# Performance work log

Measured on AMD Instinct MI355X. Metric: run time of the kernel, lower is better.

The kernel has to match this reference:

```python
import jax, jax.numpy as jnp
import numpy as np

B, S, D, H = 2, 2048, 1024, 16
DK = D // H


def setup_inputs() -> dict:
    key = jax.random.key(0)
    ks = jax.random.split(key, 9)
    def xavier(k, shape):
        fan_in, fan_out = shape[1], shape[0]
        lim = jnp.sqrt(6.0 / (fan_in + fan_out))
        return jax.random.uniform(k, shape, jnp.float32, -lim, lim)
    x = jax.random.normal(ks[0], (B, S, D), jnp.float32)
    mask = jnp.ones((B, 1, S), jnp.int32)
    Wq = xavier(ks[1], (D, D)); bq = jnp.zeros((D,), jnp.float32)
    Wk = xavier(ks[2], (D, D)); bk = jnp.zeros((D,), jnp.float32)
    Wv = xavier(ks[3], (D, D)); bv = jnp.zeros((D,), jnp.float32)
    Wo = xavier(ks[4], (D, D)); bo = jnp.zeros((D,), jnp.float32)
    return {"x": x, "mask": mask, "Wq": Wq, "bq": bq, "Wk": Wk, "bk": bk,
            "Wv": Wv, "bv": bv, "Wo": Wo, "bo": bo}


def reference(x, mask, Wq, bq, Wk, bk, Wv, bv, Wo, bo):
    # Linear layers use torch convention y = x @ W.T + b
    q = (x @ Wq.T + bq).reshape(B, S, H, DK).transpose(0, 2, 1, 3)  # [B,H,S,DK]
    k = (x @ Wk.T + bk).reshape(B, S, H, DK).transpose(0, 2, 1, 3)
    v = (x @ Wv.T + bv).reshape(B, S, H, DK).transpose(0, 2, 1, 3)
    scores = jnp.einsum('bhqd,bhkd->bhqk', q, k) / jnp.sqrt(jnp.float32(DK))
    m = mask[:, None, :, :]  # unsqueeze(1): broadcast over heads -> [B,1,1,S]
    scores = jnp.where(m == 0, jnp.float32(-1e9), scores)
    p = jax.nn.softmax(scores, axis=-1)  # dropout p=0.0 -> identity
    ctx = jnp.einsum('bhqk,bhkd->bhqd', p, v)
    ctx = ctx.transpose(0, 2, 1, 3).reshape(B, S, D)
    return ctx @ Wo.T + bo
```

## Files before the change

kernel.cpp:

```cpp
#include <hip/hip_runtime.h>
#include <hip/hip_bf16.h>
#include <math.h>

#define Bn 2
#define Sn 2048
#define Dn 1024
#define Hn 16
#define DKn 64
#define BHS (Bn * Hn * Sn)

using fragb  = __attribute__((ext_vector_type(8))) short;
using frag16 = __attribute__((ext_vector_type(8))) _Float16;
using f4     = __attribute__((ext_vector_type(4))) float;

__device__ __forceinline__ short f2bf(float f) {
    union { float f; unsigned u; } v; v.f = f;
    unsigned r = v.u + 0x7FFF + ((v.u >> 16) & 1);
    return (short)(r >> 16);
}
__device__ __forceinline__ unsigned short f2h(float f) {
    _Float16 h = (_Float16)f;
    unsigned short s; __builtin_memcpy(&s, &h, 2); return s;
}

#define GLOAD(gptr, lptr)                                                     \
    __builtin_amdgcn_global_load_lds(                                         \
        (const __attribute__((address_space(1))) unsigned int*)(const void*)(gptr), \
        (__attribute__((address_space(3))) unsigned int*)(void*)(lptr), 16, 0, 0)

#define NX (Bn * Sn * Dn)
#define NW (Dn * Dn)
#define NF4 ((NX + 4 * NW) / 4)

__global__ __launch_bounds__(256) void prep(
    const float* __restrict__ x,  const float* __restrict__ Wq,
    const float* __restrict__ Wk, const float* __restrict__ Wv,
    const float* __restrict__ Wo, const int* __restrict__ mask,
    short* __restrict__ xh,
    short* __restrict__ Wqh, short* __restrict__ Wkh,
    short* __restrict__ Wvh, short* __restrict__ Woh,
    short* __restrict__ mfb)
{
    int i = blockIdx.x * 256 + threadIdx.x;
    if (i < NF4) {
        int e = i << 2;
        const float* src; short* dst; int j;
        if (e < NX)               { src = x;  dst = xh;  j = e; }
        else if (e < NX + NW)     { src = Wq; dst = Wqh; j = e - NX; }
        else if (e < NX + 2 * NW) { src = Wk; dst = Wkh; j = e - NX - NW; }
        else if (e < NX + 3 * NW) { src = Wv; dst = Wvh; j = e - NX - 2 * NW; }
        else                      { src = Wo; dst = Woh; j = e - NX - 3 * NW; }
        float4 v = *(const float4*)(src + j);
        ushort4 o;
        o.x = f2h(v.x); o.y = f2h(v.y); o.z = f2h(v.z); o.w = f2h(v.w);
        *(ushort4*)(dst + j) = o;
    } else {
        int j = (i - NF4) << 2;
        if (j < Bn * Sn) {
            int4 m = *(const int4*)(mask + j);
            ushort4 o;
            o.x = m.x ? 0x3F80 : 0; o.y = m.y ? 0x3F80 : 0;
            o.z = m.z ? 0x3F80 : 0; o.w = m.w ? 0x3F80 : 0;
            *(ushort4*)(mfb + j) = o;
        }
    }
}


#define STAGE(kk0) do {                                                       \
    const short* _as = Asrc + (kk0);                                          \
    const short* _bs = Bsrc + (kk0);                                          \
    GLOAD(_as,            &As[wave * 512]);                                   \
    GLOAD(_as + 32 * Dn,  &As[2048 + wave * 512]);                            \
    GLOAD(_as + 64 * Dn,  &As[4096 + wave * 512]);                            \
    GLOAD(_as + 96 * Dn,  &As[6144 + wave * 512]);                            \
    GLOAD(_bs,            &Bs[wave * 512]);                                   \
    GLOAD(_bs + 32 * Dn,  &Bs[2048 + wave * 512]);                            \
    GLOAD(_bs + 64 * Dn,  &Bs[4096 + wave * 512]);                            \
    GLOAD(_bs + 96 * Dn,  &Bs[6144 + wave * 512]);                            \
} while (0)

#define COMPUTE() do {                                                        \
    frag16 _a[2][4], _b[2][4];                                                \
    _Pragma("unroll")                                                         \
    for (int kk = 0; kk < 2; kk++) {                                          \
        _Pragma("unroll")                                                     \
        for (int mi = 0; mi < 4; mi++)                                        \
            _a[kk][mi] = *(const frag16*)&As[                                 \
                (wm * 64 + mi * 16 + l16) * 64 +                              \
                (((kk << 2) | quad) ^ (l16 & 7)) * 8];                        \
        _Pragma("unroll")                                                     \
        for (int ni = 0; ni < 4; ni++)                                        \
            _b[kk][ni] = *(const frag16*)&Bs[                                 \
                (wn * 64 + ni * 16 + l16) * 64 +                              \
                (((kk << 2) | quad) ^ (l16 & 7)) * 8];                        \
    }                                                                         \
    _Pragma("unroll")                                                         \
    for (int kk = 0; kk < 2; kk++)                                            \
        _Pragma("unroll")                                                     \
        for (int mi = 0; mi < 4; mi++)                                        \
            _Pragma("unroll")                                                 \
            for (int ni = 0; ni < 4; ni++)                                    \
                acc[mi][ni] = __builtin_amdgcn_mfma_f32_16x16x32_f16(         \
                    _a[kk][mi], _b[kk][ni], acc[kk ? mi : mi][ni], 0, 0, 0);  \
} while (0)

__global__ __launch_bounds__(256) void gemm_qkv(
    const short* __restrict__ A,
    const short* __restrict__ W0, const float* __restrict__ b0,
    const short* __restrict__ W1, const float* __restrict__ b1,
    const short* __restrict__ W2, const float* __restrict__ b2,
    const int* __restrict__ mask,
    short* __restrict__ Qb, short* __restrict__ Kb, short* __restrict__ Vtb)
{
    __shared__ __align__(16) short As[128 * 64];
    __shared__ __align__(16) short Bs[128 * 64];

    const int tid  = threadIdx.x;
    const int wave = tid >> 6;
    const int lane = tid & 63;
    const int quad = lane >> 4;
    const int l16  = lane & 15;
    const int wm   = wave >> 1;
    const int wn   = wave & 1;

    const int m0   = blockIdx.y * 128;
    const int n0   = blockIdx.x * 128;
    const int widx = n0 >> 10;
    const int nl0  = n0 & 1023;

    const short* Wp   = widx == 0 ? W0 : (widx == 1 ? W1 : W2);
    const float* bias = widx == 0 ? b0 : (widx == 1 ? b1 : b2);

    f4 acc[4][4];
    #pragma unroll
    for (int i = 0; i < 4; i++)
        #pragma unroll
        for (int j = 0; j < 4; j++) {
            acc[i][j][0] = 0.f; acc[i][j][1] = 0.f;
            acc[i][j][2] = 0.f; acc[i][j][3] = 0.f;
        }

    const int sr = tid >> 3;
    const int sc = ((tid & 7) ^ (sr & 7)) * 8;
    const short* Asrc = A  + (size_t)(m0  + sr) * Dn + sc;
    const short* Bsrc = Wp + (size_t)(nl0 + sr) * Dn + sc;

    for (int k0 = 0; k0 < Dn; k0 += 64) {
        __syncthreads();
        STAGE(k0);
        __syncthreads();
        COMPUTE();
    }

    const float QSCALE = 0.125f * 1.44269504088896340736f;

    #pragma unroll
    for (int mi = 0; mi < 4; mi++) {
        #pragma unroll
        for (int ni = 0; ni < 4; ni++) {
            int nl = nl0 + wn * 64 + ni * 16 + l16;
            float bv = bias[nl];
            #pragma unroll
            for (int r = 0; r < 4; r++) {
                int m = m0 + wm * 64 + mi * 16 + quad * 4 + r;
                float v = acc[mi][ni][r] + bv;
                int b  = m >> 11, s = m & (Sn - 1);
                int h  = nl >> 6, dk = nl & 63;
                if (widx == 0)
                    Qb[((size_t)(b * Hn + h) * Sn + s) * DKn + dk] = f2bf(v * QSCALE);
                else if (widx == 1)
                    Kb[((size_t)(b * Hn + h) * Sn + s) * DKn + dk] = f2bf(v);
                else {
                    float mv = (float)mask[b * Sn + s];
                    Vtb[((size_t)(b * Hn + h) * DKn + dk) * Sn + s] = f2bf(v * mv);
                }
            }
        }
    }
}

__global__ __launch_bounds__(256) void gemm_out(
    const short* __restrict__ A, const short* __restrict__ Wp,
    const float* __restrict__ bias, float* __restrict__ outf)
{
    __shared__ __align__(16) short As[128 * 64];
    __shared__ __align__(16) short Bs[128 * 64];

    const int tid  = threadIdx.x;
    const int wave = tid >> 6;
    const int lane = tid & 63;
    const int quad = lane >> 4;
    const int l16  = lane & 15;
    const int wm   = wave >> 1;
    const int wn   = wave & 1;

    const int m0 = blockIdx.y * 128;
    const int n0 = blockIdx.x * 128;

    f4 acc[4][4];
    #pragma unroll
    for (int i = 0; i < 4; i++)
        #pragma unroll
        for (int j = 0; j < 4; j++) {
            acc[i][j][0] = 0.f; acc[i][j][1] = 0.f;
            acc[i][j][2] = 0.f; acc[i][j][3] = 0.f;
        }

    const int sr = tid >> 3;
    const int sc = ((tid & 7) ^ (sr & 7)) * 8;
    const short* Asrc = A  + (size_t)(m0 + sr) * Dn + sc;
    const short* Bsrc = Wp + (size_t)(n0 + sr) * Dn + sc;

    for (int k0 = 0; k0 < Dn; k0 += 64) {
        __syncthreads();
        STAGE(k0);
        __syncthreads();
        COMPUTE();
    }

    #pragma unroll
    for (int mi = 0; mi < 4; mi++) {
        #pragma unroll
        for (int ni = 0; ni < 4; ni++) {
            int nl = n0 + wn * 64 + ni * 16 + l16;
            float bv = bias[nl];
            #pragma unroll
            for (int r = 0; r < 4; r++) {
                int m = m0 + wm * 64 + mi * 16 + quad * 4 + r;
                outf[(size_t)m * Dn + nl] = acc[mi][ni][r] + bv;
            }
        }
    }
}

#define LP  72

__global__ __launch_bounds__(256) void attn_mfma(
    const short* __restrict__ Qb, const short* __restrict__ Kb,
    const short* __restrict__ Vtb, const short* __restrict__ mfb,
    float* __restrict__ ctxp0, float* __restrict__ ctxp1,
    float* __restrict__ lp)
{
    __shared__ __align__(16) short Ks[64 * 64];
    __shared__ __align__(16) short Vs[64 * 64];
    __shared__ short Ps[4][32 * LP];
    __shared__ __align__(16) short mfs[64];

    const int tid  = threadIdx.x;
    const int wave = tid >> 6;
    const int lane = tid & 63;
    const int quad = lane >> 4;
    const int l16  = lane & 15;

    const int split = blockIdx.x & 1;
    const int rest  = blockIdx.x >> 1;
    const int qt  = rest & 15;
    const int bhh = rest >> 4;
    const int b   = bhh >> 4;
    const int h   = bhh & 15;

    fragb qf[2][2];
    #pragma unroll
    for (int w = 0; w < 2; w++) {
        int qrow = qt * 128 + wave * 32 + w * 16 + l16;
        const short* qptr = Qb + ((size_t)bhh * Sn + qrow) * DKn + quad * 8;
        qf[w][0] = *(const fragb*)(qptr);
        qf[w][1] = *(const fragb*)(qptr + 32);
    }

    f4 ctx[2][4];
    #pragma unroll
    for (int w = 0; w < 2; w++)
        #pragma unroll
        for (int dt = 0; dt < 4; dt++) {
            ctx[w][dt][0] = 0.f; ctx[w][dt][1] = 0.f;
            ctx[w][dt][2] = 0.f; ctx[w][dt][3] = 0.f;
        }
    f4 lacc[2];
    lacc[0][0] = 0.f; lacc[0][1] = 0.f; lacc[0][2] = 0.f; lacc[0][3] = 0.f;
    lacc[1] = lacc[0];

    const int lr = lane >> 3;
    const int sc = ((lane & 7) ^ lr) * 8;
    const short* Kg = Kb  + (size_t)bhh * Sn * DKn;
    const short* Vg = Vtb + (size_t)bhh * DKn * Sn;
    const short* mg = mfb + (size_t)b * Sn;

    const short* Ksrc = Kg + (size_t)(wave * 16 + lr) * DKn + sc;
    const short* Vsrc = Vg + (size_t)(wave * 16 + lr) * Sn + sc;

    const int c0 = ((quad ^ (l16 & 7)) * 8);

    const int kt0 = split * 16;
    for (int kt = kt0; kt < kt0 + 16; kt++) {
        __syncthreads();
        GLOAD(Ksrc + (size_t)kt * 4096,             &Ks[(wave * 16) * 64]);
        GLOAD(Ksrc + (size_t)kt * 4096 + 8 * DKn,   &Ks[(wave * 16 + 8) * 64]);
        GLOAD(Vsrc + (size_t)kt * 64,               &Vs[(wave * 16) * 64]);
        GLOAD(Vsrc + (size_t)kt * 64 + 8 * Sn,      &Vs[(wave * 16 + 8) * 64]);
        if (tid < 8)
            *(uint4*)&mfs[tid * 8] = *(const uint4*)(mg + kt * 64 + tid * 8);
        __syncthreads();

        #pragma unroll
        for (int t = 0; t < 4; t++) {
            fragb k0 = *(const fragb*)&Ks[(t * 16 + l16) * 64 + c0];
            fragb k1 = *(const fragb*)&Ks[(t * 16 + l16) * 64 + (c0 ^ 32)];
            #pragma unroll
            for (int w = 0; w < 2; w++) {
                f4 a; a[0] = 0.f; a[1] = 0.f; a[2] = 0.f; a[3] = 0.f;
                a = __builtin_amdgcn_mfma_f32_16x16x32_bf16(k0, qf[w][0], a, 0, 0, 0);
                a = __builtin_amdgcn_mfma_f32_16x16x32_bf16(k1, qf[w][1], a, 0, 0, 0);
                unsigned u0 = __float_as_uint(__builtin_amdgcn_exp2f(a[0]));
                unsigned u1 = __float_as_uint(__builtin_amdgcn_exp2f(a[1]));
                unsigned u2 = __float_as_uint(__builtin_amdgcn_exp2f(a[2]));
                unsigned u3 = __float_as_uint(__builtin_amdgcn_exp2f(a[3]));
                uint2 pw;
                pw.x = __builtin_amdgcn_perm(u1, u0, 0x07060302u);
                pw.y = __builtin_amdgcn_perm(u3, u2, 0x07060302u);
                *(uint2*)&Ps[wave][(w * 16 + l16) * LP + 16 * t + quad * 4] = pw;
            }
        }

        fragb p[2][2];
        #pragma unroll
        for (int w = 0; w < 2; w++) {
            p[w][0] = *(const fragb*)&Ps[wave][(w * 16 + l16) * LP + quad * 8];
            p[w][1] = *(const fragb*)&Ps[wave][(w * 16 + l16) * LP + quad * 8 + 32];
        }
        fragb m0 = *(const fragb*)&mfs[quad * 8];
        fragb m1 = *(const fragb*)&mfs[quad * 8 + 32];
        #pragma unroll
        for (int w = 0; w < 2; w++) {
            lacc[w] = __builtin_amdgcn_mfma_f32_16x16x32_bf16(p[w][0], m0, lacc[w], 0, 0, 0);
            lacc[w] = __builtin_amdgcn_mfma_f32_16x16x32_bf16(p[w][1], m1, lacc[w], 0, 0, 0);
        }
        #pragma unroll
        for (int dt = 0; dt < 4; dt++) {
            fragb v0 = *(const fragb*)&Vs[(dt * 16 + l16) * 64 + c0];
            fragb v1 = *(const fragb*)&Vs[(dt * 16 + l16) * 64 + (c0 ^ 32)];
            #pragma unroll
            for (int w = 0; w < 2; w++) {
                ctx[w][dt] = __builtin_amdgcn_mfma_f32_16x16x32_bf16(p[w][0], v0, ctx[w][dt], 0, 0, 0);
                ctx[w][dt] = __builtin_amdgcn_mfma_f32_16x16x32_bf16(p[w][1], v1, ctx[w][dt], 0, 0, 0);
            }
        }
    }

    float* cp  = split ? ctxp1 : ctxp0;
    float* lpp = lp + (size_t)split * BHS;
    #pragma unroll
    for (int w = 0; w < 2; w++)
        #pragma unroll
        for (int r = 0; r < 4; r++) {
            int row = qt * 128 + wave * 32 + w * 16 + quad * 4 + r;
            if (l16 == 0) lpp[(size_t)bhh * Sn + row] = lacc[w][r];
            #pragma unroll
            for (int dt = 0; dt < 4; dt++)
                cp[((size_t)(b * Sn + row)) * Dn + h * DKn + dt * 16 + l16] =
                    ctx[w][dt][r];
        }
}

__global__ __launch_bounds__(256) void reduce_ctx(
    const float* __restrict__ c0, const float* __restrict__ c1,
    const float* __restrict__ lp, short* __restrict__ Ch)
{
    int i4 = blockIdx.x * 256 + threadIdx.x;
    int e    = i4 << 2;
    int brow = e >> 10;
    int d    = e & 1023;
    int b    = brow >> 11;
    int row  = brow & (Sn - 1);
    int h    = d >> 6;
    size_t li = (size_t)(b * Hn + h) * Sn + row;
    float l = lp[li] + lp[BHS + li];
    float inv = 1.f / l;
    float4 v0 = ((const float4*)c0)[i4];
    float4 v1 = ((const float4*)c1)[i4];
    ushort4 o;
    o.x = f2h((v0.x + v1.x) * inv);
    o.y = f2h((v0.y + v1.y) * inv);
    o.z = f2h((v0.z + v1.z) * inv);
    o.w = f2h((v0.w + v1.w) * inv);
    ((ushort4*)Ch)[i4] = o;
}

extern "C" void kernel_launch(void* const* d_in, const int* in_sizes, int n_in,
                              void* d_out, int out_size, void* d_ws, size_t ws_size,
                              hipStream_t stream) {
    const float* x    = (const float*)d_in[0];
    const int*   mask = (const int*)d_in[1];
    const float* Wq   = (const float*)d_in[2];
    const float* bq   = (const float*)d_in[3];
    const float* Wk   = (const float*)d_in[4];
    const float* bk   = (const float*)d_in[5];
    const float* Wv   = (const float*)d_in[6];
    const float* bv   = (const float*)d_in[7];
    const float* Wo   = (const float*)d_in[8];
    const float* bo   = (const float*)d_in[9];
    float* out = (float*)d_out;

    char* ws = (char*)d_ws;
    const size_t MB = 1024u * 1024u;
    short* xh    = (short*)(ws + 0 * MB);
    short* Wqh   = (short*)(ws + 8 * MB);
    short* Wkh   = (short*)(ws + 10 * MB);
    short* Wvh   = (short*)(ws + 12 * MB);
    short* Qb    = (short*)(ws + 16 * MB);
    short* Kb    = (short*)(ws + 24 * MB);
    short* Vtb   = (short*)(ws + 32 * MB);
    float* ctxp0 = (float*)(ws + 0 * MB);
    float* ctxp1 = (float*)(ws + 40 * MB);
    short* Woh   = (short*)(ws + 56 * MB);
    float* lp    = (float*)(ws + 58 * MB);
    short* mfb   = (short*)(ws + 59 * MB);
    short* Ch    = (short*)(ws + 60 * MB);

    const int PRE = NF4 + (Bn * Sn) / 4;
    prep<<<(PRE + 255) / 256, 256, 0, stream>>>(
        x, Wq, Wk, Wv, Wo, mask, xh, Wqh, Wkh, Wvh, Woh, mfb);

    gemm_qkv<<<dim3(24, 32), 256, 0, stream>>>(
        xh, Wqh, bq, Wkh, bk, Wvh, bv, mask, Qb, Kb, Vtb);

    attn_mfma<<<dim3(Bn * Hn * (Sn / 128) * 2), 256, 0, stream>>>(
        Qb, Kb, Vtb, mfb, ctxp0, ctxp1, lp);

    reduce_ctx<<<dim3(NX / 4 / 256), 256, 0, stream>>>(ctxp0, ctxp1, lp, Ch);

    gemm_out<<<dim3(8, 32), 256, 0, stream>>>(Ch, Woh, bo, out);
}
```

Baseline: 229.8 us.

## Double-buffer GEMM K-loop, swizzle block order, halve out-proj M tile

Both projection GEMMs now split each 64-wide K step into two 32-wide LDS buffers, so the next slice loads while the current one feeds the MFMAs, with one barrier per half step. Block indices are remapped in a grouped order to improve L2 reuse of the A and W tiles. The output GEMM uses 64x128 tiles and launches twice as many blocks, filling more CUs. The cost is more barriers per K step, and each wave does less MFMA work between syncs.

Result: no change. 229.3 us (-0.2%).

```diff
diff --git a/kernel.cpp b/kernel.cpp
--- a/kernel.cpp
+++ b/kernel.cpp
@@ -67,44 +67,6 @@
 }
 
 
-#define STAGE(kk0) do {                                                       \
-    const short* _as = Asrc + (kk0);                                          \
-    const short* _bs = Bsrc + (kk0);                                          \
-    GLOAD(_as,            &As[wave * 512]);                                   \
-    GLOAD(_as + 32 * Dn,  &As[2048 + wave * 512]);                            \
-    GLOAD(_as + 64 * Dn,  &As[4096 + wave * 512]);                            \
-    GLOAD(_as + 96 * Dn,  &As[6144 + wave * 512]);                            \
-    GLOAD(_bs,            &Bs[wave * 512]);                                   \
-    GLOAD(_bs + 32 * Dn,  &Bs[2048 + wave * 512]);                            \
-    GLOAD(_bs + 64 * Dn,  &Bs[4096 + wave * 512]);                            \
-    GLOAD(_bs + 96 * Dn,  &Bs[6144 + wave * 512]);                            \
-} while (0)
-
-#define COMPUTE() do {                                                        \
-    frag16 _a[2][4], _b[2][4];                                                \
-    _Pragma("unroll")                                                         \
-    for (int kk = 0; kk < 2; kk++) {                                          \
-        _Pragma("unroll")                                                     \
-        for (int mi = 0; mi < 4; mi++)                                        \
-            _a[kk][mi] = *(const frag16*)&As[                                 \
-                (wm * 64 + mi * 16 + l16) * 64 +                              \
-                (((kk << 2) | quad) ^ (l16 & 7)) * 8];                        \
-        _Pragma("unroll")                                                     \
-        for (int ni = 0; ni < 4; ni++)                                        \
-            _b[kk][ni] = *(const frag16*)&Bs[                                 \
-                (wn * 64 + ni * 16 + l16) * 64 +                              \
-                (((kk << 2) | quad) ^ (l16 & 7)) * 8];                        \
-    }                                                                         \
-    _Pragma("unroll")                                                         \
-    for (int kk = 0; kk < 2; kk++)                                            \
-        _Pragma("unroll")                                                     \
-        for (int mi = 0; mi < 4; mi++)                                        \
-            _Pragma("unroll")                                                 \
-            for (int ni = 0; ni < 4; ni++)                                    \
-                acc[mi][ni] = __builtin_amdgcn_mfma_f32_16x16x32_f16(         \
-                    _a[kk][mi], _b[kk][ni], acc[kk ? mi : mi][ni], 0, 0, 0);  \
-} while (0)
-
 __global__ __launch_bounds__(256) void gemm_qkv(
     const short* __restrict__ A,
     const short* __restrict__ W0, const float* __restrict__ b0,
@@ -113,8 +75,10 @@
     const int* __restrict__ mask,
     short* __restrict__ Qb, short* __restrict__ Kb, short* __restrict__ Vtb)
 {
-    __shared__ __align__(16) short As[128 * 64];
-    __shared__ __align__(16) short Bs[128 * 64];
+    __shared__ __align__(16) short As0[128 * 32];
+    __shared__ __align__(16) short Bs0[128 * 32];
+    __shared__ __align__(16) short As1[128 * 32];
+    __shared__ __align__(16) short Bs1[128 * 32];
 
     const int tid  = threadIdx.x;
     const int wave = tid >> 6;
@@ -124,8 +88,12 @@
     const int wm   = wave >> 1;
     const int wn   = wave & 1;
 
-    const int m0   = blockIdx.y * 128;
-    const int n0   = blockIdx.x * 128;
+    const int orig = blockIdx.y * 24 + blockIdx.x;
+    const int swz  = (orig & 7) * 96 + (orig >> 3);
+    const int by   = swz / 24;
+    const int bx   = swz - by * 24;
+    const int m0   = by * 128;
+    const int n0   = bx * 128;
     const int widx = n0 >> 10;
     const int nl0  = n0 & 1023;
 
@@ -141,17 +109,53 @@
             acc[i][j][2] = 0.f; acc[i][j][3] = 0.f;
         }
 
-    const int sr = tid >> 3;
-    const int sc = ((tid & 7) ^ (sr & 7)) * 8;
-    const short* Asrc = A  + (size_t)(m0  + sr) * Dn + sc;
-    const short* Bsrc = Wp + (size_t)(nl0 + sr) * Dn + sc;
-
-    for (int k0 = 0; k0 < Dn; k0 += 64) {
-        __syncthreads();
-        STAGE(k0);
-        __syncthreads();
-        COMPUTE();
-    }
+    const int K  = Dn;
+    const int r0 = tid >> 2;
+    const int sc = ((tid & 3) ^ ((tid >> 3) & 3)) * 8;
+    const short* Ar0 = A  + (size_t)(m0  + r0)      * K + sc;
+    const short* Ar1 = A  + (size_t)(m0  + r0 + 64) * K + sc;
+    const short* Br0 = Wp + (size_t)(nl0 + r0)      * K + sc;
+    const short* Br1 = Wp + (size_t)(nl0 + r0 + 64) * K + sc;
+
+    const int cA = (quad ^ ((l16 >> 1) & 3)) * 8;
+
+#define STAGEQ(AS, BS, kk) do {                                               \
+    GLOAD(Ar0 + (kk), &AS[wave * 512]);                                       \
+    GLOAD(Ar1 + (kk), &AS[2048 + wave * 512]);                                \
+    GLOAD(Br0 + (kk), &BS[wave * 512]);                                       \
+    GLOAD(Br1 + (kk), &BS[2048 + wave * 512]);                                \
+} while (0)
+
+#define COMPUTEQ(AS, BS) do {                                                 \
+    frag16 a_[4], b_[4];                                                      \
+    _Pragma("unroll")                                                         \
+    for (int mi = 0; mi < 4; mi++)                                            \
+        a_[mi] = *(const frag16*)&AS[(wm * 64 + mi * 16 + l16) * 32 + cA];    \
+    _Pragma("unroll")                                                         \
+    for (int ni = 0; ni < 4; ni++)                                            \
+        b_[ni] = *(const frag16*)&BS[(wn * 64 + ni * 16 + l16) * 32 + cA];    \
+    _Pragma("unroll")                                                         \
+    for (int mi = 0; mi < 4; mi++)                                            \
+        _Pragma("unroll")                                                     \
+        for (int ni = 0; ni < 4; ni++)                                        \
+            acc[mi][ni] = __builtin_amdgcn_mfma_f32_16x16x32_f16(             \
+                a_[mi], b_[ni], acc[mi][ni], 0, 0, 0);                        \
+} while (0)
+
+    STAGEQ(As0, Bs0, 0);
+    __syncthreads();
+    for (int k0 = 0; k0 < K - 64; k0 += 64) {
+        STAGEQ(As1, Bs1, k0 + 32);
+        COMPUTEQ(As0, Bs0);
+        __syncthreads();
+        STAGEQ(As0, Bs0, k0 + 64);
+        COMPUTEQ(As1, Bs1);
+        __syncthreads();
+    }
+    STAGEQ(As1, Bs1, K - 32);
+    COMPUTEQ(As0, Bs0);
+    __syncthreads();
+    COMPUTEQ(As1, Bs1);
 
     const float QSCALE = 0.125f * 1.44269504088896340736f;
 
@@ -184,8 +188,10 @@
     const short* __restrict__ A, const short* __restrict__ Wp,
     const float* __restrict__ bias, float* __restrict__ outf)
 {
-    __shared__ __align__(16) short As[128 * 64];
-    __shared__ __align__(16) short Bs[128 * 64];
+    __shared__ __align__(16) short As0[64 * 32];
+    __shared__ __align__(16) short Bs0[128 * 32];
+    __shared__ __align__(16) short As1[64 * 32];
+    __shared__ __align__(16) short Bs1[128 * 32];
 
     const int tid  = threadIdx.x;
     const int wave = tid >> 6;
@@ -195,39 +201,75 @@
     const int wm   = wave >> 1;
     const int wn   = wave & 1;
 
-    const int m0 = blockIdx.y * 128;
-    const int n0 = blockIdx.x * 128;
-
-    f4 acc[4][4];
-    #pragma unroll
-    for (int i = 0; i < 4; i++)
+    const int orig = blockIdx.y * 8 + blockIdx.x;
+    const int swz  = (orig & 7) * 64 + (orig >> 3);
+    const int m0   = (swz >> 3) * 64;
+    const int n0   = (swz & 7) * 128;
+
+    f4 acc[2][4];
+    #pragma unroll
+    for (int i = 0; i < 2; i++)
         #pragma unroll
         for (int j = 0; j < 4; j++) {
             acc[i][j][0] = 0.f; acc[i][j][1] = 0.f;
             acc[i][j][2] = 0.f; acc[i][j][3] = 0.f;
         }
 
-    const int sr = tid >> 3;
-    const int sc = ((tid & 7) ^ (sr & 7)) * 8;
-    const short* Asrc = A  + (size_t)(m0 + sr) * Dn + sc;
-    const short* Bsrc = Wp + (size_t)(n0 + sr) * Dn + sc;
-
-    for (int k0 = 0; k0 < Dn; k0 += 64) {
-        __syncthreads();
-        STAGE(k0);
-        __syncthreads();
-        COMPUTE();
-    }
-
-    #pragma unroll
-    for (int mi = 0; mi < 4; mi++) {
+    const int K  = Dn;
+    const int r0 = tid >> 2;
+    const int sc = ((tid & 3) ^ ((tid >> 3) & 3)) * 8;
+    const short* Ao0 = A  + (size_t)(m0 + r0)      * K + sc;
+    const short* Bo0 = Wp + (size_t)(n0 + r0)      * K + sc;
+    const short* Bo1 = Wp + (size_t)(n0 + r0 + 64) * K + sc;
+
+    const int cA = (quad ^ ((l16 >> 1) & 3)) * 8;
+
+#define STAGEO(AS, BS, kk) do {                                               \
+    GLOAD(Ao0 + (kk), &AS[wave * 512]);                                       \
+    GLOAD(Bo0 + (kk), &BS[wave * 512]);                                       \
+    GLOAD(Bo1 + (kk), &BS[2048 + wave * 512]);                                \
+} while (0)
+
+#define COMPUTEO(AS, BS) do {                                                 \
+    frag16 a_[2], b_[4];                                                      \
+    _Pragma("unroll")                                                         \
+    for (int mi = 0; mi < 2; mi++)                                            \
+        a_[mi] = *(const frag16*)&AS[(wm * 32 + mi * 16 + l16) * 32 + cA];    \
+    _Pragma("unroll")                                                         \
+    for (int ni = 0; ni < 4; ni++)                                            \
+        b_[ni] = *(const frag16*)&BS[(wn * 64 + ni * 16 + l16) * 32 + cA];    \
+    _Pragma("unroll")                                                         \
+    for (int mi = 0; mi < 2; mi++)                                            \
+        _Pragma("unroll")                                                     \
+        for (int ni = 0; ni < 4; ni++)                                        \
+            acc[mi][ni] = __builtin_amdgcn_mfma_f32_16x16x32_f16(             \
+                a_[mi], b_[ni], acc[mi][ni], 0, 0, 0);                        \
+} while (0)
+
+    STAGEO(As0, Bs0, 0);
+    __syncthreads();
+    for (int k0 = 0; k0 < K - 64; k0 += 64) {
+        STAGEO(As1, Bs1, k0 + 32);
+        COMPUTEO(As0, Bs0);
+        __syncthreads();
+        STAGEO(As0, Bs0, k0 + 64);
+        COMPUTEO(As1, Bs1);
+        __syncthreads();
+    }
+    STAGEO(As1, Bs1, K - 32);
+    COMPUTEO(As0, Bs0);
+    __syncthreads();
+    COMPUTEO(As1, Bs1);
+
+    #pragma unroll
+    for (int mi = 0; mi < 2; mi++) {
         #pragma unroll
         for (int ni = 0; ni < 4; ni++) {
             int nl = n0 + wn * 64 + ni * 16 + l16;
             float bv = bias[nl];
             #pragma unroll
             for (int r = 0; r < 4; r++) {
-                int m = m0 + wm * 64 + mi * 16 + quad * 4 + r;
+                int m = m0 + wm * 32 + mi * 16 + quad * 4 + r;
                 outf[(size_t)m * Dn + nl] = acc[mi][ni][r] + bv;
             }
         }
@@ -430,5 +472,5 @@
 
     reduce_ctx<<<dim3(NX / 4 / 256), 256, 0, stream>>>(ctxp0, ctxp1, lp, Ch);
 
-    gemm_out<<<dim3(8, 32), 256, 0, stream>>>(Ch, Woh, bo, out);
-}
+    gemm_out<<<dim3(8, 64), 256, 0, stream>>>(Ch, Woh, bo, out);
+}
```
